# Kernel tuning notes

Hardware: AMD Instinct MI355X
Metric: run time of the kernel (lower is better)

Reference implementation:

```python
import jax, jax.numpy as jnp
import numpy as np

B, C, L = 8, 512, 512
MAX_LEN = 48
LAST_WIN = 64  # hard-coded final window in the torch module


def _fofe_all(x, alpha, max_len):
    """Windowed FOFE encoder.

    Torch semantics: out[:, :, i, t] = sum_{k=0}^{w_i-1} alpha^k * x[:, :, t-1-k]
    (zero outside [0, L-1]), for windows w_i = 0..max_len-1 plus w=64,
    produced there by per-window depthwise conv1d with left pad w.
    We compute it via the linear recurrence z[t] = alpha*z[t-1] + x[t]
    (associative scan) and the windowed identity
    out_w[t] = z[t-1] - alpha^w * z[t-1-w].
    """
    Bx, Cx, Lx = x.shape
    # per-channel decay broadcast over (B, C, L)
    a = jnp.broadcast_to(alpha[None, :, 0:1], x.shape)

    def comb(c1, c2):
        a1, b1 = c1
        a2, b2 = c2
        return (a1 * a2, a2 * b1 + b2)

    _, z = jax.lax.associative_scan(comb, (a, x), axis=-1)  # z[t] = sum_k alpha^k x[t-k]

    windows_i = jnp.concatenate([jnp.arange(max_len), jnp.array([LAST_WIN])])  # (nw,)
    windows_f = windows_i.astype(x.dtype)
    W = max(max_len - 1, LAST_WIN)  # largest left shift needed
    zp = jnp.pad(z, ((0, 0), (0, 0), (W + 1, 0)))  # zeros for negative time indices

    t = jnp.arange(Lx + 1)
    base = zp[:, :, W + t]  # z[t-1], shape (B, C, L+1)
    idx = t[None, :] + (W - windows_i[:, None])  # (nw, L+1), all >= 0
    shifted = zp[:, :, idx]  # z[t-1-w], shape (B, C, nw, L+1)
    ap = jnp.power(alpha, windows_f[None, :])  # (C, nw); alpha is (C,1)
    out = base[:, :, None, :] - ap[None, :, :, None] * shifted  # (B, C, nw, L+1)
    return out


def setup_inputs() -> dict:
    key = jax.random.key(0)
    kx, = jax.random.split(key, 1)
    x = jax.random.normal(kx, (B, C, L), dtype=jnp.float32)
    alpha = jnp.full((C, 1), 0.8, dtype=jnp.float32)  # learned per-channel decay, init 0.8
    return {"x": x, "alpha": alpha, "max_len": MAX_LEN}


def reference(x, alpha, max_len):
    return _fofe_all(x, alpha, max_len)
```

## Files before the change

kernel.cpp:

```cpp
#include <hip/hip_runtime.h>


#define BB 8
#define CC 512
#define LL 512
#define NW 49
#define LO 513
#define NPAD 65

__global__ __launch_bounds__(256, 4)
void fofe_kernel(const float* __restrict__ x,
                 const float* __restrict__ alpha,
                 float* __restrict__ out)
{
    __shared__ float zp[4][LL + NPAD];

    const int tid  = threadIdx.x;
    const int wid  = tid >> 6;
    const int lane = tid & 63;
    const int row  = blockIdx.x * 2 + (wid >> 1);
    const int half = wid & 1;
    const int c    = row & (CC - 1);

    const float al = alpha[c];
    const float* xr = x + (size_t)row * LL;

    const float4 xv0 = reinterpret_cast<const float4*>(xr)[lane * 2];
    const float4 xv1 = reinterpret_cast<const float4*>(xr)[lane * 2 + 1];
    const float xe[8] = {xv0.x, xv0.y, xv0.z, xv0.w,
                         xv1.x, xv1.y, xv1.z, xv1.w};

    float l[8];
    {
        float s = 0.f;
        #pragma unroll
        for (int m = 0; m < 8; ++m) { s = fmaf(al, s, xe[m]); l[m] = s; }
    }
    float pw[8];
    {
        float p = al;
        #pragma unroll
        for (int m = 0; m < 8; ++m) { pw[m] = p; p *= al; }
    }

    float A = pw[7];
    float S = l[7];
    #pragma unroll
    for (int off = 1; off < 64; off <<= 1) {
        const float Ap = __shfl_up(A, off);
        const float Sp = __shfl_up(S, off);
        if (lane >= off) { S = fmaf(A, Sp, S); A = A * Ap; }
    }
    float carry = __shfl_up(S, 1);
    if (lane == 0) carry = 0.f;

    float* z = zp[wid];
    z[lane] = 0.f;
    if (lane == 0) z[64] = 0.f;
    #pragma unroll
    for (int m = 0; m < 8; ++m)
        z[NPAD + lane * 8 + m] = fmaf(pw[m], carry, l[m]);

    const float al2 = al * al;
    const float a4  = al2 * al2;
    const float a8  = a4 * a4;
    const float a16 = a8 * a8;
    float ap = half ? al : 1.0f;

    float* orow = out + (size_t)row * NW * LO;
    for (int i = half; i < NW; i += 2) {
        const int   w   = (i < 48) ? i : 64;
        const float apw = (i < 48) ? ap : (a16 * a16) * (a16 * a16);
        float* op = orow + (size_t)i * LO;
        const float* zb = z + (NPAD - 1);
        const float* zs = z + (NPAD - 1 - w);
        for (int t = lane; t < LO; t += 64)
            op[t] = fmaf(-apw, zs[t], zb[t]);
        ap *= al2;
    }
}

extern "C" void kernel_launch(void* const* d_in, const int* in_sizes, int n_in,
                              void* d_out, int out_size, void* d_ws, size_t ws_size,
                              hipStream_t stream)
{
    const float* x     = (const float*)d_in[0];
    const float* alpha = (const float*)d_in[1];
    float* out = (float*)d_out;

    const int rows = BB * CC;
    const int grid = rows / 2;
    fofe_kernel<<<grid, 256, 0, stream>>>(x, alpha, out);
}
```

Measured before the change: 92.35 us.

## Vectorize output stores with alignment peeling, swizzled LDS, and nontemporal writes

Result: slower. 105.4 us (+14.1%).

```diff
diff --git a/kernel.cpp b/kernel.cpp
--- a/kernel.cpp
+++ b/kernel.cpp
@@ -1,19 +1,23 @@
 #include <hip/hip_runtime.h>
 
 
-#define BB 8
 #define CC 512
 #define LL 512
 #define NW 49
 #define LO 513
 #define NPAD 65
+#define ZSZ 640
 
-__global__ __launch_bounds__(256, 4)
+typedef float f32x4 __attribute__((ext_vector_type(4)));
+
+__device__ __forceinline__ int swz(int i) { return i ^ ((i >> 5) & 3); }
+
+__global__ __launch_bounds__(256, 8)
 void fofe_kernel(const float* __restrict__ x,
                  const float* __restrict__ alpha,
                  float* __restrict__ out)
 {
-    __shared__ float zp[4][LL + NPAD];
+    __shared__ float zp[4][ZSZ];
 
     const int tid  = threadIdx.x;
     const int wid  = tid >> 6;
@@ -25,8 +29,8 @@
     const float al = alpha[c];
     const float* xr = x + (size_t)row * LL;
 
-    const float4 xv0 = reinterpret_cast<const float4*>(xr)[lane * 2];
-    const float4 xv1 = reinterpret_cast<const float4*>(xr)[lane * 2 + 1];
+    const f32x4 xv0 = reinterpret_cast<const f32x4*>(xr)[lane * 2];
+    const f32x4 xv1 = reinterpret_cast<const f32x4*>(xr)[lane * 2 + 1];
     const float xe[8] = {xv0.x, xv0.y, xv0.z, xv0.w,
                          xv1.x, xv1.y, xv1.z, xv1.w};
 
@@ -55,27 +59,50 @@
     if (lane == 0) carry = 0.f;
 
     float* z = zp[wid];
-    z[lane] = 0.f;
-    if (lane == 0) z[64] = 0.f;
+    z[swz(lane)] = 0.f;
+    if (lane == 0) z[swz(64)] = 0.f;
     #pragma unroll
     for (int m = 0; m < 8; ++m)
-        z[NPAD + lane * 8 + m] = fmaf(pw[m], carry, l[m]);
+        z[swz(NPAD + lane * 8 + m)] = fmaf(pw[m], carry, l[m]);
 
     const float al2 = al * al;
     const float a4  = al2 * al2;
     const float a8  = a4 * a4;
     const float a16 = a8 * a8;
+    const float a64 = (a16 * a16) * (a16 * a16);
     float ap = half ? al : 1.0f;
 
-    float* orow = out + (size_t)row * NW * LO;
+    float* orow = out + (size_t)row * (NW * LO);
+
     for (int i = half; i < NW; i += 2) {
         const int   w   = (i < 48) ? i : 64;
-        const float apw = (i < 48) ? ap : (a16 * a16) * (a16 * a16);
-        float* op = orow + (size_t)i * LO;
-        const float* zb = z + (NPAD - 1);
-        const float* zs = z + (NPAD - 1 - w);
-        for (int t = lane; t < LO; t += 64)
-            op[t] = fmaf(-apw, zs[t], zb[t]);
+        const float apw = (i < 48) ? ap : a64;
+        float* op = orow + i * LO;
+        const int q    = (row + i) & 3;
+        const int peel = (4 - q) & 3;
+        const int zb0  = NPAD - 1;
+
+        if (lane < peel) {
+            const int t = lane;
+            op[t] = fmaf(-apw, z[swz(zb0 + t - w)], z[swz(zb0 + t)]);
+        }
+
+        const int nf4  = (LO - peel) >> 2;
+        const int tail = (LO - peel) & 3;
+        for (int f = lane; f < nf4; f += 64) {
+            const int t0 = peel + 4 * f;
+            f32x4 v;
+            v.x = fmaf(-apw, z[swz(zb0 + t0     - w)], z[swz(zb0 + t0    )]);
+            v.y = fmaf(-apw, z[swz(zb0 + t0 + 1 - w)], z[swz(zb0 + t0 + 1)]);
+            v.z = fmaf(-apw, z[swz(zb0 + t0 + 2 - w)], z[swz(zb0 + t0 + 2)]);
+            v.w = fmaf(-apw, z[swz(zb0 + t0 + 3 - w)], z[swz(zb0 + t0 + 3)]);
+            __builtin_nontemporal_store(v, reinterpret_cast<f32x4*>(op + t0));
+        }
+
+        if (lane < tail) {
+            const int t = peel + 4 * nf4 + lane;
+            op[t] = fmaf(-apw, z[swz(zb0 + t - w)], z[swz(zb0 + t)]);
+        }
         ap *= al2;
     }
 }
@@ -88,7 +115,7 @@
     const float* alpha = (const float*)d_in[1];
     float* out = (float*)d_out;
 
-    const int rows = BB * CC;
+    const int rows = 8 * CC;
     const int grid = rows / 2;
     fofe_kernel<<<grid, 256, 0, stream>>>(x, alpha, out);
 }
```

## Compute FOFE windows by direct accumulation with 4-wide vector stores

Applied to the files above, without the earlier changes.

New measurement: 97.55 us. 5.6% more time.

```diff
diff --git a/kernel.cpp b/kernel.cpp
--- a/kernel.cpp
+++ b/kernel.cpp
@@ -1,19 +1,23 @@
 #include <hip/hip_runtime.h>
 
 
-#define BB 8
 #define CC 512
 #define LL 512
 #define NW 49
 #define LO 513
-#define NPAD 65
+#define PAD 68
+#define XSZ 592
 
-__global__ __launch_bounds__(256, 4)
+typedef float f32x4 __attribute__((ext_vector_type(4)));
+
+__device__ __forceinline__ int swz(int i) { return i ^ ((i >> 5) & 3); }
+
+__global__ __launch_bounds__(256, 8)
 void fofe_kernel(const float* __restrict__ x,
                  const float* __restrict__ alpha,
                  float* __restrict__ out)
 {
-    __shared__ float zp[4][LL + NPAD];
+    __shared__ float xs[4][XSZ];
 
     const int tid  = threadIdx.x;
     const int wid  = tid >> 6;
@@ -24,60 +28,79 @@
 
     const float al = alpha[c];
     const float* xr = x + (size_t)row * LL;
+    float* xw = xs[wid];
 
-    const float4 xv0 = reinterpret_cast<const float4*>(xr)[lane * 2];
-    const float4 xv1 = reinterpret_cast<const float4*>(xr)[lane * 2 + 1];
-    const float xe[8] = {xv0.x, xv0.y, xv0.z, xv0.w,
-                         xv1.x, xv1.y, xv1.z, xv1.w};
+    for (int k = lane; k < PAD; k += 64) xw[swz(k)] = 0.f;
+    for (int k = lane; k < LL;  k += 64) xw[swz(PAD + k)] = xr[k];
 
-    float l[8];
-    {
-        float s = 0.f;
+    const int t0 = half ? (257 + 4 * lane) : (4 * lane);
+
+    float w0 = xw[swz(PAD + t0 - 1)];
+    float w1 = xw[swz(PAD + t0)];
+    float w2 = xw[swz(PAD + t0 + 1)];
+    float w3 = xw[swz(PAD + t0 + 2)];
+
+    f32x4 acc = {0.f, 0.f, 0.f, 0.f};
+    float apj = 1.0f;
+    const float a2 = al * al, a3 = a2 * al, a4 = a2 * a2;
+
+    float* op = out + (size_t)row * (NW * LO) + t0;
+
+#define ROWSTEP(P, A, B, C, D)                                   \
+    { f32x4 tv = acc; __builtin_memcpy(op, &tv, 16); op += LO;   \
+      acc.x = fmaf((P), (A), acc.x); acc.y = fmaf((P), (B), acc.y); \
+      acc.z = fmaf((P), (C), acc.z); acc.w = fmaf((P), (D), acc.w); }
+#define ACCSTEP(P, A, B, C, D)                                   \
+    { acc.x = fmaf((P), (A), acc.x); acc.y = fmaf((P), (B), acc.y); \
+      acc.z = fmaf((P), (C), acc.z); acc.w = fmaf((P), (D), acc.w); }
+
+    for (int jb = 0; jb < 48; jb += 4) {
+        const int ib = PAD + t0 - 2 - jb;
+        const float n1 = xw[swz(ib)];
+        const float n2 = xw[swz(ib - 1)];
+        const float n3 = xw[swz(ib - 2)];
+        const float n4 = xw[swz(ib - 3)];
+        const float p1 = apj * al, p2 = apj * a2, p3 = apj * a3;
+        ROWSTEP(apj, w0, w1, w2, w3)
+        ROWSTEP(p1,  n1, w0, w1, w2)
+        ROWSTEP(p2,  n2, n1, w0, w1)
+        ROWSTEP(p3,  n3, n2, n1, w0)
+        apj *= a4;
+        w0 = n4; w1 = n3; w2 = n2; w3 = n1;
+    }
+    for (int jb = 48; jb < 64; jb += 4) {
+        const int ib = PAD + t0 - 2 - jb;
+        const float n1 = xw[swz(ib)];
+        const float n2 = xw[swz(ib - 1)];
+        const float n3 = xw[swz(ib - 2)];
+        const float n4 = xw[swz(ib - 3)];
+        const float p1 = apj * al, p2 = apj * a2, p3 = apj * a3;
+        ACCSTEP(apj, w0, w1, w2, w3)
+        ACCSTEP(p1,  n1, w0, w1, w2)
+        ACCSTEP(p2,  n2, n1, w0, w1)
+        ACCSTEP(p3,  n3, n2, n1, w0)
+        apj *= a4;
+        w0 = n4; w1 = n3; w2 = n2; w3 = n1;
+    }
+    { f32x4 tv = acc; __builtin_memcpy(op, &tv, 16); }
+
+    if (half == 0) {
+        float pl = 1.f, mm = al;
         #pragma unroll
-        for (int m = 0; m < 8; ++m) { s = fmaf(al, s, xe[m]); l[m] = s; }
+        for (int b = 0; b < 6; ++b) { pl = (lane & (1 << b)) ? pl * mm : pl; mm *= mm; }
+        float s = pl * xw[swz(PAD + 255 - lane)];
+        #pragma unroll
+        for (int off = 1; off < 64; off <<= 1) {
+            const float v = __shfl_up(s, off);
+            if (lane >= off) s += v;
+        }
+        float* ocol = out + (size_t)row * (NW * LO) + 256;
+        if (lane <= 46) ocol[(size_t)(lane + 1) * LO] = s;
+        if (lane == 47) ocol[0] = 0.f;
+        if (lane == 63) ocol[(size_t)48 * LO] = s;
     }
-    float pw[8];
-    {
-        float p = al;
-        #pragma unroll
-        for (int m = 0; m < 8; ++m) { pw[m] = p; p *= al; }
-    }
-
-    float A = pw[7];
-    float S = l[7];
-    #pragma unroll
-    for (int off = 1; off < 64; off <<= 1) {
-        const float Ap = __shfl_up(A, off);
-        const float Sp = __shfl_up(S, off);
-        if (lane >= off) { S = fmaf(A, Sp, S); A = A * Ap; }
-    }
-    float carry = __shfl_up(S, 1);
-    if (lane == 0) carry = 0.f;
-
-    float* z = zp[wid];
-    z[lane] = 0.f;
-    if (lane == 0) z[64] = 0.f;
-    #pragma unroll
-    for (int m = 0; m < 8; ++m)
-        z[NPAD + lane * 8 + m] = fmaf(pw[m], carry, l[m]);
-
-    const float al2 = al * al;
-    const float a4  = al2 * al2;
-    const float a8  = a4 * a4;
-    const float a16 = a8 * a8;
-    float ap = half ? al : 1.0f;
-
-    float* orow = out + (size_t)row * NW * LO;
-    for (int i = half; i < NW; i += 2) {
-        const int   w   = (i < 48) ? i : 64;
-        const float apw = (i < 48) ? ap : (a16 * a16) * (a16 * a16);
-        float* op = orow + (size_t)i * LO;
-        const float* zb = z + (NPAD - 1);
-        const float* zs = z + (NPAD - 1 - w);
-        for (int t = lane; t < LO; t += 64)
-            op[t] = fmaf(-apw, zs[t], zb[t]);
-        ap *= al2;
-    }
+#undef ROWSTEP
+#undef ACCSTEP
 }
 
 extern "C" void kernel_launch(void* const* d_in, const int* in_sizes, int n_in,
@@ -88,7 +111,7 @@
     const float* alpha = (const float*)d_in[1];
     float* out = (float*)d_out;
 
-    const int rows = BB * CC;
+    const int rows = 8 * CC;
     const int grid = rows / 2;
     fofe_kernel<<<grid, 256, 0, stream>>>(x, alpha, out);
 }
```

## Flatten block output into aligned float4 stores with swizzled LDS and power LUT

Applied to the files above, without the earlier changes.

Result: slower. 115.7 us (+25.3%).

```diff
diff --git a/kernel.cpp b/kernel.cpp
--- a/kernel.cpp
+++ b/kernel.cpp
@@ -1,82 +1,127 @@
 #include <hip/hip_runtime.h>
 
 
-#define BB 8
 #define CC 512
 #define LL 512
 #define NW 49
 #define LO 513
-#define NPAD 65
+#define SLAB (NW * LO)
+#define R0F (2 * SLAB)
+#define ZOFF 69
+#define ZROW 640
 
-__global__ __launch_bounds__(256, 4)
+typedef float f32x4 __attribute__((ext_vector_type(4)));
+
+__device__ __forceinline__ int swz(int i) { return i ^ ((i >> 5) & 3); }
+
+__global__ __launch_bounds__(256)
 void fofe_kernel(const float* __restrict__ x,
                  const float* __restrict__ alpha,
                  float* __restrict__ out)
 {
-    __shared__ float zp[4][LL + NPAD];
+    __shared__ float zs[2][ZROW];
+    __shared__ float lut[2][NW];
 
     const int tid  = threadIdx.x;
     const int wid  = tid >> 6;
     const int lane = tid & 63;
-    const int row  = blockIdx.x * 2 + (wid >> 1);
-    const int half = wid & 1;
-    const int c    = row & (CC - 1);
+    const int blk  = blockIdx.x;
 
-    const float al = alpha[c];
-    const float* xr = x + (size_t)row * LL;
+    if (wid < 2) {
+        const int row = blk * 2 + wid;
+        const float al = alpha[row & (CC - 1)];
+        const float* xr = x + (size_t)row * LL;
 
-    const float4 xv0 = reinterpret_cast<const float4*>(xr)[lane * 2];
-    const float4 xv1 = reinterpret_cast<const float4*>(xr)[lane * 2 + 1];
-    const float xe[8] = {xv0.x, xv0.y, xv0.z, xv0.w,
-                         xv1.x, xv1.y, xv1.z, xv1.w};
+        const f32x4 xv0 = reinterpret_cast<const f32x4*>(xr)[lane * 2];
+        const f32x4 xv1 = reinterpret_cast<const f32x4*>(xr)[lane * 2 + 1];
+        const float xe[8] = {xv0.x, xv0.y, xv0.z, xv0.w,
+                             xv1.x, xv1.y, xv1.z, xv1.w};
+        float l[8];
+        {
+            float s = 0.f;
+            #pragma unroll
+            for (int m = 0; m < 8; ++m) { s = fmaf(al, s, xe[m]); l[m] = s; }
+        }
+        float pw[8];
+        {
+            float p = al;
+            #pragma unroll
+            for (int m = 0; m < 8; ++m) { pw[m] = p; p *= al; }
+        }
+        float A = pw[7], S = l[7];
+        #pragma unroll
+        for (int off = 1; off < 64; off <<= 1) {
+            const float Ap = __shfl_up(A, off);
+            const float Sp = __shfl_up(S, off);
+            if (lane >= off) { S = fmaf(A, Sp, S); A = A * Ap; }
+        }
+        float carry = __shfl_up(S, 1);
+        if (lane == 0) carry = 0.f;
 
-    float l[8];
-    {
-        float s = 0.f;
+        float* z = zs[wid];
+        z[swz(lane)] = 0.f;
+        if (lane < ZOFF - 64) z[swz(64 + lane)] = 0.f;
+        if (lane < 11) z[swz(ZOFF + LL + lane)] = 0.f;
         #pragma unroll
-        for (int m = 0; m < 8; ++m) { s = fmaf(al, s, xe[m]); l[m] = s; }
+        for (int m = 0; m < 8; ++m)
+            z[swz(ZOFF + lane * 8 + m)] = fmaf(pw[m], carry, l[m]);
     }
-    float pw[8];
-    {
-        float p = al;
+    if (tid < 2 * NW) {
+        const int r = tid / NW, i = tid - r * NW;
+        const int row = blk * 2 + r;
+        const float al = alpha[row & (CC - 1)];
+        const int w = (i < 48) ? i : 64;
+        float p = 1.f, m = al;
         #pragma unroll
-        for (int m = 0; m < 8; ++m) { pw[m] = p; p *= al; }
+        for (int b = 0; b < 7; ++b) { if (w & (1 << b)) p *= m; m *= m; }
+        lut[r][i] = p;
     }
+    __syncthreads();
 
-    float A = pw[7];
-    float S = l[7];
-    #pragma unroll
-    for (int off = 1; off < 64; off <<= 1) {
-        const float Ap = __shfl_up(A, off);
-        const float Sp = __shfl_up(S, off);
-        if (lane >= off) { S = fmaf(A, Sp, S); A = A * Ap; }
-    }
-    float carry = __shfl_up(S, 1);
-    if (lane == 0) carry = 0.f;
+    float* base = out + (size_t)blk * R0F;
+    const int peel = (4 - ((2 * blk) & 3)) & 3;
+    const int nf4  = (R0F - peel) >> 2;
+    const int ntail = (R0F - peel) & 3;
 
-    float* z = zp[wid];
-    z[lane] = 0.f;
-    if (lane == 0) z[64] = 0.f;
-    #pragma unroll
-    for (int m = 0; m < 8; ++m)
-        z[NPAD + lane * 8 + m] = fmaf(pw[m], carry, l[m]);
+    auto eval1 = [&](int e) -> float {
+        const int r01 = (e >= SLAB);
+        const int e2  = e - r01 * SLAB;
+        const unsigned i = (unsigned)e2 / 513u;
+        const int t   = e2 - (int)i * 513;
+        const int w   = (i < 48u) ? (int)i : 64;
+        return fmaf(-lut[r01][i], zs[r01][swz(ZOFF - 1 + t - w)],
+                    zs[r01][swz(ZOFF - 1 + t)]);
+    };
 
-    const float al2 = al * al;
-    const float a4  = al2 * al2;
-    const float a8  = a4 * a4;
-    const float a16 = a8 * a8;
-    float ap = half ? al : 1.0f;
+    if (tid < peel)          base[tid] = eval1(tid);
+    if (tid < ntail)         base[peel + 4 * nf4 + tid] = eval1(peel + 4 * nf4 + tid);
 
-    float* orow = out + (size_t)row * NW * LO;
-    for (int i = half; i < NW; i += 2) {
-        const int   w   = (i < 48) ? i : 64;
-        const float apw = (i < 48) ? ap : (a16 * a16) * (a16 * a16);
-        float* op = orow + (size_t)i * LO;
-        const float* zb = z + (NPAD - 1);
-        const float* zs = z + (NPAD - 1 - w);
-        for (int t = lane; t < LO; t += 64)
-            op[t] = fmaf(-apw, zs[t], zb[t]);
-        ap *= al2;
+    for (int f = tid; f < nf4; f += 256) {
+        const int el  = peel + 4 * f;
+        const int r01 = (el >= SLAB);
+        const int e2  = el - r01 * SLAB;
+        const unsigned i = (unsigned)e2 / 513u;
+        const int t   = e2 - (int)i * 513;
+
+        if (t <= 509) {
+            const float apw = lut[r01][i];
+            const float* z = zs[r01];
+            const int k0 = ZOFF - 1 + t;
+            const int w  = (i < 48u) ? (int)i : 64;
+            f32x4 v;
+            v.x = fmaf(-apw, z[swz(k0     - w)], z[swz(k0    )]);
+            v.y = fmaf(-apw, z[swz(k0 + 1 - w)], z[swz(k0 + 1)]);
+            v.z = fmaf(-apw, z[swz(k0 + 2 - w)], z[swz(k0 + 2)]);
+            v.w = fmaf(-apw, z[swz(k0 + 3 - w)], z[swz(k0 + 3)]);
+            *reinterpret_cast<f32x4*>(base + el) = v;
+        } else {
+            f32x4 v;
+            v.x = eval1(el);
+            v.y = eval1(el + 1);
+            v.z = eval1(el + 2);
+            v.w = eval1(el + 3);
+            *reinterpret_cast<f32x4*>(base + el) = v;
+        }
     }
 }
 
@@ -88,7 +133,6 @@
     const float* alpha = (const float*)d_in[1];
     float* out = (float*)d_out;
 
-    const int rows = BB * CC;
-    const int grid = rows / 2;
+    const int grid = (8 * CC) / 2;
     fofe_kernel<<<grid, 256, 0, stream>>>(x, alpha, out);
 }
```
